# Optimization experiments

Hardware: AMD Instinct MI355X
Metric: run time of the kernel (lower is better)

## Reference

```python
import jax, jax.numpy as jnp
import numpy as np

N_NODES = 100000
N_EDGES = 1600000
NFEAT = 128
NHID = 64
DROPOUT = 0.5


def setup_inputs() -> dict:
    key = jax.random.key(0)
    k1, k2, k3, k4, k5, k6 = jax.random.split(key, 6)
    x = jax.random.normal(k1, (N_NODES, NFEAT), dtype=jnp.float32)
    edge_row = jax.random.randint(k2, (N_EDGES,), 0, N_NODES, dtype=jnp.int32)
    edge_col = jax.random.randint(k3, (N_EDGES,), 0, N_NODES, dtype=jnp.int32)
    edge_val = jax.random.uniform(k4, (N_EDGES,), dtype=jnp.float32)
    # GraphConvolution params (uniform init as in Kipf's reference impl)
    stdv = 1.0 / np.sqrt(NHID)
    W = jax.random.uniform(k5, (NFEAT, NHID), minval=-stdv, maxval=stdv, dtype=jnp.float32)
    b = jax.random.uniform(k6, (NHID,), minval=-stdv, maxval=stdv, dtype=jnp.float32)
    return {"x": x, "edge_row": edge_row, "edge_col": edge_col,
            "edge_val": edge_val, "W": W, "b": b}


def reference(x, edge_row, edge_col, edge_val, W, b):
    # GraphConvolution: support = x @ W ; out = spmm(adj, support) + b
    support = x @ W                                   # [N, nhid]
    msgs = edge_val[:, None] * support[edge_col]       # gather: [E, nhid]
    agg = jax.ops.segment_sum(msgs, edge_row, num_segments=N_NODES)  # scatter-add
    h = jax.nn.relu(agg + b)
    # F.dropout(p=0.5, training=True): inverted dropout with fixed mask
    keep = 1.0 - DROPOUT
    mask = jax.random.bernoulli(jax.random.key(42), keep, h.shape)
    return jnp.where(mask, h / keep, 0.0)
```

## Files before the change

kernel.cpp:

```cpp
#include <hip/hip_runtime.h>

#define N_NODES 100000
#define N_EDGES 1600000
#define NFEAT 128
#define NHID 64

#define BBITS 8
#define NBUCK 391
#define BATCH 4096
#define NBATCH ((N_EDGES + BATCH - 1) / BATCH)
#define STRIDE 4608
#define CMASK 0x1FFFF

typedef __attribute__((ext_vector_type(8))) short short8;
typedef __attribute__((ext_vector_type(4))) float f32x4;

__device__ __forceinline__ unsigned short f2bf(float f) {
  unsigned u = __float_as_uint(f);
  u += 0x7fffu + ((u >> 16) & 1u);
  return (unsigned short)(u >> 16);
}

__global__ __launch_bounds__(256) void gcn_wt(const float* __restrict__ W,
                                              unsigned short* __restrict__ wt,
                                              int* __restrict__ cursor) {
  const int i = blockIdx.x * 256 + threadIdx.x;
  const int n = i >> 7;
  const int k = i & 127;
  wt[i] = f2bf(W[k * NHID + n]);
  if (blockIdx.x == 0)
    for (int b = threadIdx.x; b < NBUCK; b += 256)
      cursor[b * 16] = b * STRIDE;
}

__global__ __launch_bounds__(256) void gcn_gemm(const float* __restrict__ x,
                                                const unsigned short* __restrict__ wt,
                                                unsigned short* __restrict__ support_h) {
  __shared__ float ldsx[64 * NFEAT];
  const int t = threadIdx.x;
  const int node0 = blockIdx.x * 64;
  const float4* __restrict__ gx = (const float4*)(x + (size_t)node0 * NFEAT);
  float4* lx4 = (float4*)ldsx;
  const int limit4 = (N_NODES - node0) * (NFEAT / 4);
#pragma unroll
  for (int i = 0; i < 8; ++i) {
    const int idx = i * 256 + t;
    if (idx < limit4) lx4[idx] = gx[idx];
  }
  __syncthreads();
  const int wv = t >> 6;
  const int lane = t & 63;
  const int quad = lane >> 4;
  const int nl = lane & 15;
  const int mrow = wv * 16 + nl;
  f32x4 acc[4];
#pragma unroll
  for (int nt = 0; nt < 4; ++nt)
#pragma unroll
    for (int r = 0; r < 4; ++r) acc[nt][r] = 0.f;
#pragma unroll
  for (int kc = 0; kc < 4; ++kc) {
    const float* ap = &ldsx[mrow * NFEAT + kc * 32 + quad * 8];
    const float4 a0 = *(const float4*)ap;
    const float4 a1 = *(const float4*)(ap + 4);
    union { short8 v; unsigned short s[8]; } au;
    au.s[0] = f2bf(a0.x); au.s[1] = f2bf(a0.y);
    au.s[2] = f2bf(a0.z); au.s[3] = f2bf(a0.w);
    au.s[4] = f2bf(a1.x); au.s[5] = f2bf(a1.y);
    au.s[6] = f2bf(a1.z); au.s[7] = f2bf(a1.w);
#pragma unroll
    for (int nt = 0; nt < 4; ++nt) {
      const short8 bf = *(const short8*)(wt + (size_t)(nt * 16 + nl) * NFEAT +
                                         kc * 32 + quad * 8);
      acc[nt] = __builtin_amdgcn_mfma_f32_16x16x32_bf16(au.v, bf, acc[nt], 0, 0, 0);
    }
  }
#pragma unroll
  for (int nt = 0; nt < 4; ++nt)
#pragma unroll
    for (int r = 0; r < 4; ++r) {
      const int node = node0 + wv * 16 + quad * 4 + r;
      if (node < N_NODES)
        support_h[(size_t)node * NHID + nt * 16 + nl] = f2bf(acc[nt][r]);
    }
}

__global__ __launch_bounds__(512) void gcn_bin(const int* __restrict__ erow,
                                               const int* __restrict__ ecol,
                                               const float* __restrict__ eval_,
                                               int* __restrict__ cursor,
                                               int2* __restrict__ eg) {
  __shared__ int h[NBUCK];
  __shared__ int ofs[NBUCK];
  __shared__ int sm[512];
  __shared__ int spx[BATCH];
  __shared__ int sv[BATCH];
  __shared__ short sb[BATCH];
  const int t = threadIdx.x;
  if (t < NBUCK) h[t] = 0;
  __syncthreads();
  const int base = blockIdx.x * BATCH;
  const int n = min(BATCH, N_EDGES - base);
  int mypx[8], myv[8], myrank[8], myb[8];
#pragma unroll
  for (int u = 0; u < 8; ++u) {
    const int j = t + u * 512;
    if (j < n) {
      const int r = erow[base + j];
      mypx[u] = ((r & 255) << 17) | ecol[base + j];
      myv[u] = __float_as_int(eval_[base + j]);
      myb[u] = r >> BBITS;
      myrank[u] = atomicAdd(&h[myb[u]], 1);
    }
  }
  __syncthreads();
  const int hv = (t < NBUCK) ? h[t] : 0;
  sm[t] = hv;
  __syncthreads();
  for (int off = 1; off < 512; off <<= 1) {
    const int xv = (t >= off) ? sm[t - off] : 0;
    __syncthreads();
    sm[t] += xv;
    __syncthreads();
  }
  if (t < NBUCK) ofs[t] = sm[t] - hv;
  __syncthreads();
#pragma unroll
  for (int u = 0; u < 8; ++u) {
    const int j = t + u * 512;
    if (j < n) {
      const int pos = ofs[myb[u]] + myrank[u];
      spx[pos] = mypx[u];
      sv[pos] = myv[u];
      sb[pos] = (short)myb[u];
    }
  }
  if (t < NBUCK) {
    const int c = h[t];
    if (c > 0) {
      const int gb = atomicAdd(&cursor[t * 16], c);
      h[t] = gb - ofs[t];
    }
  }
  __syncthreads();
  for (int j = t; j < n; j += 512) {
    const int d = h[sb[j]] + j;
    eg[d] = make_int2(spx[j], sv[j]);
  }
}

__global__ __launch_bounds__(512) void gcn_rowsort(const int* __restrict__ cursor,
                                                   int2* __restrict__ eg,
                                                   int2* __restrict__ rs_re) {
  __shared__ int cnt[256];
  __shared__ int sm[256];
  __shared__ int rofs[256];
  const int t = threadIdx.x;
  const int k = blockIdx.x;
  const int bbase = k * STRIDE;
  const int n = cursor[k * 16] - bbase;
  if (t < 256) cnt[t] = 0;
  __syncthreads();
  int px[9], pv[9], rk[9];
#pragma unroll
  for (int u = 0; u < 9; ++u) {
    const int j = t + u * 512;
    if (j < n) {
      const int2 p = eg[bbase + j];
      px[u] = p.x;
      pv[u] = p.y;
      rk[u] = atomicAdd(&cnt[((unsigned)p.x) >> 17], 1);
    }
  }
  __syncthreads();
  const int myc = (t < 256) ? cnt[t] : 0;
  if (t < 256) sm[t] = myc;
  __syncthreads();
  for (int off = 1; off < 256; off <<= 1) {
    int xv = 0;
    if (t >= off && t < 256) xv = sm[t - off];
    __syncthreads();
    if (t < 256) sm[t] += xv;
    __syncthreads();
  }
  if (t < 256) {
    rofs[t] = sm[t] - myc;
    const int node = (k << BBITS) + t;
    const int start = bbase + sm[t] - myc;
    if (node < N_NODES) rs_re[node] = make_int2(start, start + myc);
  }
  __syncthreads();
#pragma unroll
  for (int u = 0; u < 9; ++u) {
    const int j = t + u * 512;
    if (j < n) {
      const int d = bbase + rofs[px[u] >> 17] + rk[u];
      eg[d] = make_int2(px[u] & CMASK, pv[u]);
    }
  }
}

__device__ __forceinline__ unsigned rotl32(unsigned v, int r) {
  return (v << r) | (v >> (32 - r));
}

__device__ __forceinline__ unsigned threefry_draw(unsigned i) {
  const unsigned ks0 = 0u;
  const unsigned ks1 = 42u;
  const unsigned ks2 = 0x1BD11BDAu ^ 42u;
  unsigned x0 = 0u + ks0;
  unsigned x1 = i + ks1;
#define TF_ROUND(r) { x0 += x1; x1 = rotl32(x1, (r)); x1 ^= x0; }
  TF_ROUND(13) TF_ROUND(15) TF_ROUND(26) TF_ROUND(6)
  x0 += ks1; x1 += ks2 + 1u;
  TF_ROUND(17) TF_ROUND(29) TF_ROUND(16) TF_ROUND(24)
  x0 += ks2; x1 += ks0 + 2u;
  TF_ROUND(13) TF_ROUND(15) TF_ROUND(26) TF_ROUND(6)
  x0 += ks0; x1 += ks1 + 3u;
  TF_ROUND(17) TF_ROUND(29) TF_ROUND(16) TF_ROUND(24)
  x0 += ks1; x1 += ks2 + 4u;
  TF_ROUND(13) TF_ROUND(15) TF_ROUND(26) TF_ROUND(6)
  x0 += ks2; x1 += ks0 + 5u;
#undef TF_ROUND
  return x0 ^ x1;
}

__global__ __launch_bounds__(256) void gcn_aggregate(const int2* __restrict__ rs_re,
                                                     const int2* __restrict__ eg,
                                                     const unsigned short* __restrict__ support_h,
                                                     const float* __restrict__ b,
                                                     float* __restrict__ out) {
  const int node = (int)((blockIdx.x * 256u + threadIdx.x) >> 6);
  const int lane = threadIdx.x & 63;
  const int grp = lane >> 3;
  const int sub = lane & 7;
  const int2 se = rs_re[node];
  const int s = se.x;
  const int e = se.y;
  float acc[8];
#pragma unroll
  for (int j = 0; j < 8; ++j) acc[j] = 0.f;
  for (int i = s; i < e; i += 8) {
    const int idx = i + grp;
    const int2 p = (idx < e) ? eg[idx] : make_int2(0, 0);
    const uint4 q = ((const uint4*)support_h)[(size_t)p.x * 8 + sub];
    const float v = __int_as_float(p.y);
    acc[0] = __builtin_fmaf(v, __uint_as_float(q.x << 16), acc[0]);
    acc[1] = __builtin_fmaf(v, __uint_as_float(q.x & 0xffff0000u), acc[1]);
    acc[2] = __builtin_fmaf(v, __uint_as_float(q.y << 16), acc[2]);
    acc[3] = __builtin_fmaf(v, __uint_as_float(q.y & 0xffff0000u), acc[3]);
    acc[4] = __builtin_fmaf(v, __uint_as_float(q.z << 16), acc[4]);
    acc[5] = __builtin_fmaf(v, __uint_as_float(q.z & 0xffff0000u), acc[5]);
    acc[6] = __builtin_fmaf(v, __uint_as_float(q.w << 16), acc[6]);
    acc[7] = __builtin_fmaf(v, __uint_as_float(q.w & 0xffff0000u), acc[7]);
  }
  const int g0 = grp & 1, g1 = (grp >> 1) & 1, g2 = grp >> 2;
  float v4[4];
#pragma unroll
  for (int i = 0; i < 4; ++i) {
    const float keep = g0 ? acc[2 * i + 1] : acc[2 * i];
    const float give = g0 ? acc[2 * i] : acc[2 * i + 1];
    v4[i] = keep + __shfl_xor(give, 8);
  }
  float v2[2];
#pragma unroll
  for (int i = 0; i < 2; ++i) {
    const float keep = g1 ? v4[2 * i + 1] : v4[2 * i];
    const float give = g1 ? v4[2 * i] : v4[2 * i + 1];
    v2[i] = keep + __shfl_xor(give, 16);
  }
  const float keep = g2 ? v2[1] : v2[0];
  const float give = g2 ? v2[0] : v2[1];
  const float aval = keep + __shfl_xor(give, 32);
  const int feat = (sub << 3) | grp;
  const float h = fmaxf(aval + b[feat], 0.f);
  const unsigned idxg = (unsigned)node * 64u + (unsigned)feat;
  const bool keepm = (threefry_draw(idxg) >> 31) == 0u;
  out[idxg] = keepm ? h * 2.0f : 0.0f;
}

extern "C" void kernel_launch(void* const* d_in, const int* in_sizes, int n_in,
                              void* d_out, int out_size, void* d_ws, size_t ws_size,
                              hipStream_t stream) {
  const float* x     = (const float*)d_in[0];
  const int*   erow  = (const int*)d_in[1];
  const int*   ecol  = (const int*)d_in[2];
  const float* eval_ = (const float*)d_in[3];
  const float* W     = (const float*)d_in[4];
  const float* b     = (const float*)d_in[5];
  float* out = (float*)d_out;

  char* ws = (char*)d_ws;
  unsigned short* support_h = (unsigned short*)(ws);
  unsigned short* wt        = (unsigned short*)(ws + 12800000);
  int2* rs_re   = (int2*)(ws + 12816384);
  int*  cursor  = (int*)(ws + 13616384);
  int2* eg      = (int2*)(ws + 13641472);

  hipLaunchKernelGGL(gcn_wt, dim3(32), dim3(256), 0, stream, W, wt, cursor);
  hipLaunchKernelGGL(gcn_gemm, dim3((N_NODES + 63) / 64), dim3(256), 0, stream,
                     x, wt, support_h);
  hipLaunchKernelGGL(gcn_bin, dim3(NBATCH), dim3(512), 0, stream,
                     erow, ecol, eval_, cursor, eg);
  hipLaunchKernelGGL(gcn_rowsort, dim3(NBUCK), dim3(512), 0, stream,
                     cursor, eg, rs_re);
  hipLaunchKernelGGL(gcn_aggregate, dim3(N_NODES / 4), dim3(256), 0, stream,
                     rs_re, eg, support_h, b, out);
}
```

Before: 207.8 us.

## Fuse per-row sort into aggregation using LDS-local CSR and replicated bucket cursors

Removes the separate rowsort kernel. The aggregation kernel now loads each bucket's edges, counting-sorts them by row in shared memory, and aggregates directly from LDS. This saves a global write and re-read of the edge array plus one launch. Bucket cursors are split into 4 replicas to reduce atomic contention, and the block-wide scan in the binning kernel becomes a wave-shuffle scan. The trade-offs are fixed capacity limits (1536 per replica, 2560 per half-bucket) that could overflow with skewed inputs, and fewer, larger aggregation blocks (782), which lowers parallelism.

```diff
diff --git a/kernel.cpp b/kernel.cpp
--- a/kernel.cpp
+++ b/kernel.cpp
@@ -9,7 +9,9 @@
 #define NBUCK 391
 #define BATCH 4096
 #define NBATCH ((N_EDGES + BATCH - 1) / BATCH)
-#define STRIDE 4608
+#define NREP 4
+#define RSTRIDE 1536
+#define HCAP 2560
 #define CMASK 0x1FFFF
 
 typedef __attribute__((ext_vector_type(8))) short short8;
@@ -29,8 +31,8 @@
   const int k = i & 127;
   wt[i] = f2bf(W[k * NHID + n]);
   if (blockIdx.x == 0)
-    for (int b = threadIdx.x; b < NBUCK; b += 256)
-      cursor[b * 16] = b * STRIDE;
+    for (int b = threadIdx.x; b < NBUCK * NREP; b += 256)
+      cursor[b * 16] = 0;
 }
 
 __global__ __launch_bounds__(256) void gcn_gemm(const float* __restrict__ x,
@@ -92,11 +94,12 @@
                                                int2* __restrict__ eg) {
   __shared__ int h[NBUCK];
   __shared__ int ofs[NBUCK];
-  __shared__ int sm[512];
+  __shared__ int wsum[8];
   __shared__ int spx[BATCH];
   __shared__ int sv[BATCH];
   __shared__ short sb[BATCH];
   const int t = threadIdx.x;
+  const int rep = blockIdx.x & (NREP - 1);
   if (t < NBUCK) h[t] = 0;
   __syncthreads();
   const int base = blockIdx.x * BATCH;
@@ -115,15 +118,27 @@
   }
   __syncthreads();
   const int hv = (t < NBUCK) ? h[t] : 0;
-  sm[t] = hv;
-  __syncthreads();
-  for (int off = 1; off < 512; off <<= 1) {
-    const int xv = (t >= off) ? sm[t - off] : 0;
-    __syncthreads();
-    sm[t] += xv;
-    __syncthreads();
-  }
-  if (t < NBUCK) ofs[t] = sm[t] - hv;
+  const int lane = t & 63;
+  int v = hv;
+#pragma unroll
+  for (int off = 1; off < 64; off <<= 1) {
+    const int u = __shfl_up(v, off);
+    if (lane >= off) v += u;
+  }
+  if (lane == 63) wsum[t >> 6] = v;
+  __syncthreads();
+  int wbase = 0;
+  const int mywv = t >> 6;
+  for (int w = 0; w < mywv; ++w) wbase += wsum[w];
+  const int my_ofs = wbase + v - hv;
+  if (t < NBUCK) {
+    ofs[t] = my_ofs;
+    const int c = hv;
+    if (c > 0) {
+      const int old = atomicAdd(&cursor[(t * NREP + rep) * 16], c);
+      h[t] = (t * NREP + rep) * RSTRIDE + old - my_ofs;
+    }
+  }
   __syncthreads();
 #pragma unroll
   for (int u = 0; u < 8; ++u) {
@@ -135,68 +150,10 @@
       sb[pos] = (short)myb[u];
     }
   }
-  if (t < NBUCK) {
-    const int c = h[t];
-    if (c > 0) {
-      const int gb = atomicAdd(&cursor[t * 16], c);
-      h[t] = gb - ofs[t];
-    }
-  }
   __syncthreads();
   for (int j = t; j < n; j += 512) {
     const int d = h[sb[j]] + j;
     eg[d] = make_int2(spx[j], sv[j]);
-  }
-}
-
-__global__ __launch_bounds__(512) void gcn_rowsort(const int* __restrict__ cursor,
-                                                   int2* __restrict__ eg,
-                                                   int2* __restrict__ rs_re) {
-  __shared__ int cnt[256];
-  __shared__ int sm[256];
-  __shared__ int rofs[256];
-  const int t = threadIdx.x;
-  const int k = blockIdx.x;
-  const int bbase = k * STRIDE;
-  const int n = cursor[k * 16] - bbase;
-  if (t < 256) cnt[t] = 0;
-  __syncthreads();
-  int px[9], pv[9], rk[9];
-#pragma unroll
-  for (int u = 0; u < 9; ++u) {
-    const int j = t + u * 512;
-    if (j < n) {
-      const int2 p = eg[bbase + j];
-      px[u] = p.x;
-      pv[u] = p.y;
-      rk[u] = atomicAdd(&cnt[((unsigned)p.x) >> 17], 1);
-    }
-  }
-  __syncthreads();
-  const int myc = (t < 256) ? cnt[t] : 0;
-  if (t < 256) sm[t] = myc;
-  __syncthreads();
-  for (int off = 1; off < 256; off <<= 1) {
-    int xv = 0;
-    if (t >= off && t < 256) xv = sm[t - off];
-    __syncthreads();
-    if (t < 256) sm[t] += xv;
-    __syncthreads();
-  }
-  if (t < 256) {
-    rofs[t] = sm[t] - myc;
-    const int node = (k << BBITS) + t;
-    const int start = bbase + sm[t] - myc;
-    if (node < N_NODES) rs_re[node] = make_int2(start, start + myc);
-  }
-  __syncthreads();
-#pragma unroll
-  for (int u = 0; u < 9; ++u) {
-    const int j = t + u * 512;
-    if (j < n) {
-      const int d = bbase + rofs[px[u] >> 17] + rk[u];
-      eg[d] = make_int2(px[u] & CMASK, pv[u]);
-    }
   }
 }
 
@@ -225,58 +182,120 @@
   return x0 ^ x1;
 }
 
-__global__ __launch_bounds__(256) void gcn_aggregate(const int2* __restrict__ rs_re,
-                                                     const int2* __restrict__ eg,
-                                                     const unsigned short* __restrict__ support_h,
-                                                     const float* __restrict__ b,
-                                                     float* __restrict__ out) {
-  const int node = (int)((blockIdx.x * 256u + threadIdx.x) >> 6);
-  const int lane = threadIdx.x & 63;
+__global__ __launch_bounds__(512) void gcn_rowagg(const int* __restrict__ cursor,
+                                                  const int2* __restrict__ eg,
+                                                  const unsigned short* __restrict__ support_h,
+                                                  const float* __restrict__ b,
+                                                  float* __restrict__ out) {
+  __shared__ int2 srec[HCAP];
+  __shared__ int cnt[128];
+  __shared__ int rstart[128];
+  const int t = threadIdx.x;
+  const int k = blockIdx.x >> 1;
+  const int half = blockIdx.x & 1;
+  if (t < 128) cnt[t] = 0;
+  __syncthreads();
+  int px[12], pv[12], rk[12];
+  int idx = 0;
+#pragma unroll
+  for (int rep = 0; rep < NREP; ++rep) {
+    const int span = k * NREP + rep;
+    const int n = cursor[span * 16];
+    const int sbase = span * RSTRIDE;
+#pragma unroll
+    for (int u = 0; u < 3; ++u, ++idx) {
+      const int j = t + u * 512;
+      const bool ok = j < n;
+      int2 p = make_int2(0, 0);
+      if (ok) p = eg[sbase + j];
+      px[idx] = p.x;
+      pv[idx] = p.y;
+      const int r = ((unsigned)p.x) >> 17;
+      rk[idx] = (ok && ((r >> 7) == half)) ? atomicAdd(&cnt[r & 127], 1) : -1;
+    }
+  }
+  __syncthreads();
+  if (t < 64) {
+    const int a0 = cnt[t];
+    const int a1 = cnt[64 + t];
+    int s0 = a0;
+#pragma unroll
+    for (int off = 1; off < 64; off <<= 1) {
+      const int u = __shfl_up(s0, off);
+      if (t >= off) s0 += u;
+    }
+    const int tot0 = __shfl(s0, 63);
+    int s1 = a1;
+#pragma unroll
+    for (int off = 1; off < 64; off <<= 1) {
+      const int u = __shfl_up(s1, off);
+      if (t >= off) s1 += u;
+    }
+    rstart[t] = s0 - a0;
+    rstart[64 + t] = tot0 + s1 - a1;
+  }
+  __syncthreads();
+#pragma unroll
+  for (int u = 0; u < 12; ++u) {
+    if (rk[u] >= 0) {
+      const int r = (((unsigned)px[u]) >> 17) & 127;
+      srec[rstart[r] + rk[u]] = make_int2(px[u] & CMASK, pv[u]);
+    }
+  }
+  __syncthreads();
+  const int wv = t >> 6;
+  const int lane = t & 63;
   const int grp = lane >> 3;
   const int sub = lane & 7;
-  const int2 se = rs_re[node];
-  const int s = se.x;
-  const int e = se.y;
-  float acc[8];
-#pragma unroll
-  for (int j = 0; j < 8; ++j) acc[j] = 0.f;
-  for (int i = s; i < e; i += 8) {
-    const int idx = i + grp;
-    const int2 p = (idx < e) ? eg[idx] : make_int2(0, 0);
-    const uint4 q = ((const uint4*)support_h)[(size_t)p.x * 8 + sub];
-    const float v = __int_as_float(p.y);
-    acc[0] = __builtin_fmaf(v, __uint_as_float(q.x << 16), acc[0]);
-    acc[1] = __builtin_fmaf(v, __uint_as_float(q.x & 0xffff0000u), acc[1]);
-    acc[2] = __builtin_fmaf(v, __uint_as_float(q.y << 16), acc[2]);
-    acc[3] = __builtin_fmaf(v, __uint_as_float(q.y & 0xffff0000u), acc[3]);
-    acc[4] = __builtin_fmaf(v, __uint_as_float(q.z << 16), acc[4]);
-    acc[5] = __builtin_fmaf(v, __uint_as_float(q.z & 0xffff0000u), acc[5]);
-    acc[6] = __builtin_fmaf(v, __uint_as_float(q.w << 16), acc[6]);
-    acc[7] = __builtin_fmaf(v, __uint_as_float(q.w & 0xffff0000u), acc[7]);
-  }
-  const int g0 = grp & 1, g1 = (grp >> 1) & 1, g2 = grp >> 2;
-  float v4[4];
-#pragma unroll
-  for (int i = 0; i < 4; ++i) {
-    const float keep = g0 ? acc[2 * i + 1] : acc[2 * i];
-    const float give = g0 ? acc[2 * i] : acc[2 * i + 1];
-    v4[i] = keep + __shfl_xor(give, 8);
-  }
-  float v2[2];
-#pragma unroll
-  for (int i = 0; i < 2; ++i) {
-    const float keep = g1 ? v4[2 * i + 1] : v4[2 * i];
-    const float give = g1 ? v4[2 * i] : v4[2 * i + 1];
-    v2[i] = keep + __shfl_xor(give, 16);
-  }
-  const float keep = g2 ? v2[1] : v2[0];
-  const float give = g2 ? v2[0] : v2[1];
-  const float aval = keep + __shfl_xor(give, 32);
   const int feat = (sub << 3) | grp;
-  const float h = fmaxf(aval + b[feat], 0.f);
-  const unsigned idxg = (unsigned)node * 64u + (unsigned)feat;
-  const bool keepm = (threefry_draw(idxg) >> 31) == 0u;
-  out[idxg] = keepm ? h * 2.0f : 0.0f;
+  const float bias = b[feat];
+  for (int rr = 0; rr < 16; ++rr) {
+    const int r = wv * 16 + rr;
+    const int node = (k << BBITS) + (half << 7) + r;
+    if (node >= N_NODES) break;
+    const int s = rstart[r];
+    const int e = s + cnt[r];
+    float acc[8];
+#pragma unroll
+    for (int j = 0; j < 8; ++j) acc[j] = 0.f;
+    for (int i = s; i < e; i += 8) {
+      const int ii = i + grp;
+      int2 p = make_int2(0, 0);
+      if (ii < e) p = srec[ii];
+      const uint4 q = ((const uint4*)support_h)[(size_t)p.x * 8 + sub];
+      const float v = __int_as_float(p.y);
+      acc[0] = __builtin_fmaf(v, __uint_as_float(q.x << 16), acc[0]);
+      acc[1] = __builtin_fmaf(v, __uint_as_float(q.x & 0xffff0000u), acc[1]);
+      acc[2] = __builtin_fmaf(v, __uint_as_float(q.y << 16), acc[2]);
+      acc[3] = __builtin_fmaf(v, __uint_as_float(q.y & 0xffff0000u), acc[3]);
+      acc[4] = __builtin_fmaf(v, __uint_as_float(q.z << 16), acc[4]);
+      acc[5] = __builtin_fmaf(v, __uint_as_float(q.z & 0xffff0000u), acc[5]);
+      acc[6] = __builtin_fmaf(v, __uint_as_float(q.w << 16), acc[6]);
+      acc[7] = __builtin_fmaf(v, __uint_as_float(q.w & 0xffff0000u), acc[7]);
+    }
+    const int g0 = grp & 1, g1 = (grp >> 1) & 1, g2 = grp >> 2;
+    float v4[4];
+#pragma unroll
+    for (int i = 0; i < 4; ++i) {
+      const float keep = g0 ? acc[2 * i + 1] : acc[2 * i];
+      const float give = g0 ? acc[2 * i] : acc[2 * i + 1];
+      v4[i] = keep + __shfl_xor(give, 8);
+    }
+    float v2[2];
+#pragma unroll
+    for (int i = 0; i < 2; ++i) {
+      const float keep = g1 ? v4[2 * i + 1] : v4[2 * i];
+      const float give = g1 ? v4[2 * i] : v4[2 * i + 1];
+      v2[i] = keep + __shfl_xor(give, 16);
+    }
+    const float keep = g2 ? v2[1] : v2[0];
+    const float give = g2 ? v2[0] : v2[1];
+    const float aval = keep + __shfl_xor(give, 32);
+    const float h = fmaxf(aval + bias, 0.f);
+    const unsigned idxg = (unsigned)node * 64u + (unsigned)feat;
+    const bool keepm = (threefry_draw(idxg) >> 31) == 0u;
+    out[idxg] = keepm ? h * 2.0f : 0.0f;
+  }
 }
 
 extern "C" void kernel_launch(void* const* d_in, const int* in_sizes, int n_in,
@@ -293,17 +312,14 @@
   char* ws = (char*)d_ws;
   unsigned short* support_h = (unsigned short*)(ws);
   unsigned short* wt        = (unsigned short*)(ws + 12800000);
-  int2* rs_re   = (int2*)(ws + 12816384);
-  int*  cursor  = (int*)(ws + 13616384);
-  int2* eg      = (int2*)(ws + 13641472);
+  int*  cursor  = (int*)(ws + 12816384);
+  int2* eg      = (int2*)(ws + 12916480);
 
   hipLaunchKernelGGL(gcn_wt, dim3(32), dim3(256), 0, stream, W, wt, cursor);
   hipLaunchKernelGGL(gcn_gemm, dim3((N_NODES + 63) / 64), dim3(256), 0, stream,
                      x, wt, support_h);
   hipLaunchKernelGGL(gcn_bin, dim3(NBATCH), dim3(512), 0, stream,
                      erow, ecol, eval_, cursor, eg);
-  hipLaunchKernelGGL(gcn_rowsort, dim3(NBUCK), dim3(512), 0, stream,
-                     cursor, eg, rs_re);
-  hipLaunchKernelGGL(gcn_aggregate, dim3(N_NODES / 4), dim3(256), 0, stream,
-                     rs_re, eg, support_h, b, out);
-}
+  hipLaunchKernelGGL(gcn_rowagg, dim3(2 * NBUCK), dim3(512), 0, stream,
+                     cursor, eg, support_h, b, out);
+}
```

After: 194.0 us. -6.6%, faster.
